# Optimization experiments

Measured on AMD Instinct MI355X. Metric: run time of the kernel, lower is better.

Reference implementation:

```python
import jax, jax.numpy as jnp
import numpy as np

N, IN_DIM, HID, HEADS, HOPS, NCLS, E = 20000, 1536, 256, 4, 3, 3, 320000
HD = HID // HEADS
EPS = 1e-5
NEG_SLOPE = 0.2


def layer_norm(x, g, b):
    mu = jnp.mean(x, axis=-1, keepdims=True)
    var = jnp.var(x, axis=-1, keepdims=True)
    return (x - mu) * jax.lax.rsqrt(var + EPS) * g + b


def gatv2(x, src, dst, Wl, bl, Wr, br, att, bias):
    # x: [N, HID]; src/dst: [E'] (self loops included)
    xl = (x @ Wl + bl).reshape(N, HEADS, HD)  # source transform
    xr = (x @ Wr + br).reshape(N, HEADS, HD)  # target transform
    e = jax.nn.leaky_relu(xl[src] + xr[dst], NEG_SLOPE)          # [E', H, D]
    logits = jnp.einsum('ehd,hd->eh', e, att)                     # [E', H]
    m = jax.ops.segment_max(logits, dst, num_segments=N)         # [N, H]
    ex = jnp.exp(logits - m[dst])
    denom = jax.ops.segment_sum(ex, dst, num_segments=N)
    alpha = ex / denom[dst]                                       # softmax per dst
    msg = xl[src] * alpha[:, :, None]                             # [E', H, D]
    out = jax.ops.segment_sum(msg, dst, num_segments=N)
    return out.reshape(N, HID) + bias


def setup_inputs() -> dict:
    key = jax.random.key(0)
    ks = jax.random.split(key, 20)
    s = lambda k, shp, sc: jax.random.normal(k, shp, jnp.float32) * sc
    return {
        'features': s(ks[0], (N, IN_DIM), 1.0),
        'edge_index': jax.random.randint(ks[1], (2, E), 0, N, jnp.int64),
        'proj_W': s(ks[2], (IN_DIM, HID), 0.02),
        'proj_b': jnp.zeros((HID,), jnp.float32),
        'n0_g': jnp.ones((HID,), jnp.float32),
        'n0_b': jnp.zeros((HID,), jnp.float32),
        'Wl': s(ks[3], (HOPS, HID, HID), 0.05),
        'bl': jnp.zeros((HOPS, HID), jnp.float32),
        'Wr': s(ks[4], (HOPS, HID, HID), 0.05),
        'br': jnp.zeros((HOPS, HID), jnp.float32),
        'att': s(ks[5], (HOPS, HEADS, HD), 0.1),
        'gbias': jnp.zeros((HOPS, HID), jnp.float32),
        'ln_g': jnp.ones((HOPS, HID), jnp.float32),
        'ln_b': jnp.zeros((HOPS, HID), jnp.float32),
        'h1_W': s(ks[6], (HID, HID), 0.05),
        'h1_b': jnp.zeros((HID,), jnp.float32),
        'h2_W': s(ks[7], (HID, NCLS), 0.05),
        'h2_b': jnp.zeros((NCLS,), jnp.float32),
    }


def reference(features, edge_index, proj_W, proj_b, n0_g, n0_b, Wl, bl, Wr, br,
              att, gbias, ln_g, ln_b, h1_W, h1_b, h2_W, h2_b):
    # add self loops (PyG GATv2Conv default)
    loop = jnp.arange(N, dtype=edge_index.dtype)
    src = jnp.concatenate([edge_index[0], loop])
    dst = jnp.concatenate([edge_index[1], loop])

    x = layer_norm(features @ proj_W + proj_b, n0_g, n0_b)
    for h in range(HOPS):
        g = gatv2(x, src, dst, Wl[h], bl[h], Wr[h], br[h], att[h], gbias[h])
        x = layer_norm(g + x, ln_g[h], ln_b[h])
    # head (dropout inactive at eval); torch GELU is exact erf form
    x = jax.nn.gelu(x @ h1_W + h1_b, approximate=False)
    return x @ h2_W + h2_b
```

## Files before the change

### kernel.cpp

```cpp
#include <hip/hip_runtime.h>
#include <hip/hip_bf16.h>
#include <math.h>

#define NN 20000
#define MPAD 20096
#define INDIM 1536
#define HID 256
#define NE 320000
#define NEDGE (NE + NN)
#define EPSV 1e-5f
#define NEG 0.2f

typedef unsigned short ushort_b;
typedef unsigned int uint32;
typedef __bf16 bf16x8 __attribute__((ext_vector_type(8)));
typedef float f32x4 __attribute__((ext_vector_type(4)));

#define AS1(p) ((const __attribute__((address_space(1))) void*)(p))
#define AS3(p) ((__attribute__((address_space(3))) void*)(p))

__device__ inline ushort_b f2bf(float x) {
  union { float f; uint32 u; } v; v.f = x;
  uint32 r = v.u + 0x7FFFu + ((v.u >> 16) & 1u);
  return (ushort_b)(r >> 16);
}
__device__ inline float bf2f(ushort_b h) {
  union { uint32 u; float f; } v; v.u = ((uint32)h) << 16;
  return v.f;
}
__device__ inline float4 ldbf4(const ushort_b* p) {
  ushort4 u = *(const ushort4*)p;
  float4 f;
  f.x = bf2f(u.x); f.y = bf2f(u.y); f.z = bf2f(u.z); f.w = bf2f(u.w);
  return f;
}

template<int AFP32, int OUTMODE, int SPLITK>
__global__ __launch_bounds__(256) void gemm_mfma(
    const void* __restrict__ Av,
    const ushort_b* __restrict__ Bt0, const ushort_b* __restrict__ Bt1,
    const float* __restrict__ bias0, const float* __restrict__ bias1,
    void* __restrict__ C0, void* __restrict__ C1,
    int Mstore, int Kloop, int Kstride)
{
  __shared__ ushort_b As0[128 * 32], As1[128 * 32];
  __shared__ ushort_b Bs0[128 * 32], Bs1[128 * 32];
  const ushort_b* Bt;
  const float* bias;
  void* Cv;
  int kbase;
  if (SPLITK > 1) {
    Bt = Bt0;
    bias = (blockIdx.z == 0) ? bias0 : nullptr;
    Cv = (float*)C0 + (size_t)blockIdx.z * NN * HID;
    kbase = blockIdx.z * Kloop;
  } else {
    Bt = blockIdx.z ? Bt1 : Bt0;
    bias = blockIdx.z ? bias1 : bias0;
    Cv = blockIdx.z ? C1 : C0;
    kbase = 0;
  }

  int tid = threadIdx.x;
  int wave = tid >> 6, lane = tid & 63;
  int r0 = blockIdx.y * 128;
  int c0 = blockIdx.x * 128;
  int wm = (wave >> 1) << 6, wn = (wave & 1) << 6;
  int mrow = lane & 15, quad = lane >> 4;
  int nk = Kloop >> 5;

  const float* Af = (const float*)Av;
  const ushort_b* Ab = (const ushort_b*)Av;

  f32x4 acc[4][4] = {};
  float4 pA0[4], pA1[4];

  auto issueB = [&](int k0, ushort_b* lds) {
#pragma unroll
    for (int it = 0; it < 2; it++) {
      int off = (wave << 10) + (it << 12) + (lane << 4);
      int row = off >> 6, colb = off & 63;
      const char* g = (const char*)Bt + ((size_t)(c0 + row) * Kstride + kbase + k0) * 2 + colb;
      __builtin_amdgcn_global_load_lds(AS1(g), AS3((char*)lds + off), 16, 0, 0);
    }
  };
  auto issueA = [&](int k0, ushort_b* lds) {
#pragma unroll
    for (int it = 0; it < 2; it++) {
      int off = (wave << 10) + (it << 12) + (lane << 4);
      int row = off >> 6, colb = off & 63;
      const char* g = (const char*)Ab + ((size_t)(r0 + row) * Kstride + kbase + k0) * 2 + colb;
      __builtin_amdgcn_global_load_lds(AS1(g), AS3((char*)lds + off), 16, 0, 0);
    }
  };
  auto loadA = [&](int k0, float4* dst) {
#pragma unroll
    for (int p = 0; p < 4; p++) {
      int off4 = (p << 8) + tid;
      int row = off4 >> 3, col4 = off4 & 7;
      int grow = r0 + row;
      dst[p] = (grow < Mstore)
          ? *(const float4*)(Af + (size_t)grow * Kstride + kbase + k0 + (col4 << 2))
          : make_float4(0.f, 0.f, 0.f, 0.f);
    }
  };
  auto writeA = [&](const float4* src, ushort_b* lds) {
#pragma unroll
    for (int p = 0; p < 4; p++) {
      int off4 = (p << 8) + tid;
      int row = off4 >> 3, col4 = off4 & 7;
      uint2 u;
      u.x = (uint32)f2bf(src[p].x) | ((uint32)f2bf(src[p].y) << 16);
      u.y = (uint32)f2bf(src[p].z) | ((uint32)f2bf(src[p].w) << 16);
      *(uint2*)(lds + (row << 5) + (col4 << 2)) = u;
    }
  };
  auto computeStage = [&](const ushort_b* Asb, const ushort_b* Bsb) {
    bf16x8 af[4], bfr[4];
#pragma unroll
    for (int t = 0; t < 4; t++) {
      af[t]  = *(const bf16x8*)(Asb + ((wm + (t << 4) + mrow) << 5) + (quad << 3));
      bfr[t] = *(const bf16x8*)(Bsb + ((wn + (t << 4) + mrow) << 5) + (quad << 3));
    }
#pragma unroll
    for (int mt = 0; mt < 4; mt++)
#pragma unroll
      for (int nt = 0; nt < 4; nt++)
        acc[mt][nt] = __builtin_amdgcn_mfma_f32_16x16x32_bf16(af[mt], bfr[nt], acc[mt][nt], 0, 0, 0);
  };

  if (AFP32) {
    loadA(0, pA0);
    issueB(0, Bs0);
    loadA(32, pA1);
    writeA(pA0, As0);
  } else {
    issueA(0, As0);
    issueB(0, Bs0);
  }

  for (int k = 0; k < nk; k += 2) {
    __syncthreads();
    if (k + 1 < nk) {
      issueB((k + 1) << 5, Bs1);
      if (AFP32) {
        writeA(pA1, As1);
        if (k + 2 < nk) loadA((k + 2) << 5, pA0);
      } else {
        issueA((k + 1) << 5, As1);
      }
    }
    computeStage(As0, Bs0);
    __syncthreads();
    if (k + 2 < nk) {
      issueB((k + 2) << 5, Bs0);
      if (AFP32) {
        writeA(pA0, As0);
        if (k + 3 < nk) loadA((k + 3) << 5, pA1);
      } else {
        issueA((k + 2) << 5, As0);
      }
    }
    computeStage(As1, Bs1);
  }

#pragma unroll
  for (int nt = 0; nt < 4; nt++) {
    int col = c0 + wn + (nt << 4) + mrow;
    float bb = bias ? bias[col] : 0.f;
#pragma unroll
    for (int mt = 0; mt < 4; mt++) {
#pragma unroll
      for (int r = 0; r < 4; r++) {
        int row = r0 + wm + (mt << 4) + (quad << 2) + r;
        if (row < Mstore) {
          float v = acc[mt][nt][r] + bb;
          if (OUTMODE == 3) v = 0.5f * v * (1.f + erff(v * 0.70710678118654752f));
          if (OUTMODE == 0) ((float*)Cv)[(size_t)row * 256 + col] = v;
          else              ((ushort_b*)Cv)[(size_t)row * 256 + col] = f2bf(v);
        }
      }
    }
  }
}

__global__ __launch_bounds__(256) void transpose_all(
    const float* __restrict__ Wl, const float* __restrict__ Wr,
    const float* __restrict__ h1W, const float* __restrict__ projW,
    ushort_b* __restrict__ wbase, ushort_b* __restrict__ wtp)
{
  __shared__ float t[32][33];
  int z = blockIdx.z;
  int tx = threadIdx.x;
  if (z < 7) {
    const float* in = (z < 3) ? Wl + (size_t)z * 65536
                    : (z < 6) ? Wr + (size_t)(z - 3) * 65536
                              : h1W;
    ushort_b* out = wbase + (size_t)z * 65536;
    int bx = blockIdx.x * 32, by = blockIdx.y * 32;
    for (int i = threadIdx.y; i < 32; i += 8)
      t[i][tx] = in[(size_t)(by + i) * 256 + bx + tx];
    __syncthreads();
    for (int i = threadIdx.y; i < 32; i += 8)
      out[(size_t)(bx + i) * 256 + by + tx] = f2bf(t[tx][i]);
  } else {
    if (blockIdx.y) return;
    int by = (z - 7) * 32;
    int bx = blockIdx.x * 32;
    for (int i = threadIdx.y; i < 32; i += 8)
      t[i][tx] = projW[(size_t)(by + i) * 256 + bx + tx];
    __syncthreads();
    for (int i = threadIdx.y; i < 32; i += 8)
      wtp[(size_t)(bx + i) * INDIM + by + tx] = f2bf(t[tx][i]);
  }
}

__global__ __launch_bounds__(256) void ln_sum4_kernel(
    const float* __restrict__ parts, const float* __restrict__ g,
    const float* __restrict__ b, float* __restrict__ out,
    ushort_b* __restrict__ bf_out)
{
  int wave = threadIdx.x >> 6, lane = threadIdx.x & 63;
  int row = blockIdx.x * 4 + wave;
  int c = lane << 2;
  if (row >= NN) {
    if (row < MPAD) *(ushort4*)(bf_out + (size_t)row * HID + c) = make_ushort4(0, 0, 0, 0);
    return;
  }
  float4 v = *(const float4*)(parts + (size_t)row * HID + c);
#pragma unroll
  for (int k = 1; k < 4; k++) {
    float4 p = *(const float4*)(parts + (size_t)k * NN * HID + (size_t)row * HID + c);
    v.x += p.x; v.y += p.y; v.z += p.z; v.w += p.w;
  }
  float s1 = v.x + v.y + v.z + v.w;
  float s2 = v.x * v.x + v.y * v.y + v.z * v.z + v.w * v.w;
#pragma unroll
  for (int m = 1; m < 64; m <<= 1) {
    s1 += __shfl_xor(s1, m, 64);
    s2 += __shfl_xor(s2, m, 64);
  }
  float mu = s1 * (1.f / 256.f);
  float var = s2 * (1.f / 256.f) - mu * mu;
  float rstd = rsqrtf(var + EPSV);
  float4 gv = *(const float4*)(g + c);
  float4 bv = *(const float4*)(b + c);
  float4 o;
  o.x = (v.x - mu) * rstd * gv.x + bv.x;
  o.y = (v.y - mu) * rstd * gv.y + bv.y;
  o.z = (v.z - mu) * rstd * gv.z + bv.z;
  o.w = (v.w - mu) * rstd * gv.w + bv.w;
  *(float4*)(out + (size_t)row * HID + c) = o;
  ushort4 ub;
  ub.x = f2bf(o.x); ub.y = f2bf(o.y); ub.z = f2bf(o.z); ub.w = f2bf(o.w);
  *(ushort4*)(bf_out + (size_t)row * HID + c) = ub;
}

__global__ void count_kernel(const int* __restrict__ ei, int* __restrict__ cnt)
{
  int e = blockIdx.x * blockDim.x + threadIdx.x;
  if (e < NEDGE) {
    int d = (e < NE) ? ei[NE + e] : (e - NE);
    atomicAdd(&cnt[d], 1);
  }
}

__global__ __launch_bounds__(1024) void scan_kernel(
    const int* __restrict__ cnt, int* __restrict__ offs, int* __restrict__ cursor)
{
  __shared__ int sums[1024];
  int tid = threadIdx.x;
  const int CH = 20;
  int base = tid * CH;
  int loc[CH];
  int s = 0;
#pragma unroll
  for (int i = 0; i < CH; i++) {
    int idx = base + i;
    int v = (idx < NN) ? cnt[idx] : 0;
    loc[i] = s;
    s += v;
  }
  sums[tid] = s;
  __syncthreads();
  for (int off = 1; off < 1024; off <<= 1) {
    int t = (tid >= off) ? sums[tid - off] : 0;
    __syncthreads();
    sums[tid] += t;
    __syncthreads();
  }
  int pre = (tid == 0) ? 0 : sums[tid - 1];
#pragma unroll
  for (int i = 0; i < CH; i++) {
    int idx = base + i;
    if (idx < NN) { int e = pre + loc[i]; offs[idx] = e; cursor[idx] = e; }
  }
  if (tid == 0) offs[NN] = NEDGE;
}

__global__ void scatter_kernel(const int* __restrict__ ei, int* __restrict__ cursor,
                               int* __restrict__ csr_src)
{
  int e = blockIdx.x * blockDim.x + threadIdx.x;
  if (e < NEDGE) {
    int s, d;
    if (e < NE) { s = ei[e]; d = ei[NE + e]; }
    else { s = e - NE; d = e - NE; }
    int p = atomicAdd(&cursor[d], 1);
    csr_src[p] = s;
  }
}

__device__ inline float edge_logit(float4 xv, float4 xrv, float4 attv) {
  float e0 = xv.x + xrv.x, e1 = xv.y + xrv.y, e2 = xv.z + xrv.z, e3 = xv.w + xrv.w;
  e0 = (e0 > 0.f) ? e0 : NEG * e0;
  e1 = (e1 > 0.f) ? e1 : NEG * e1;
  e2 = (e2 > 0.f) ? e2 : NEG * e2;
  e3 = (e3 > 0.f) ? e3 : NEG * e3;
  float lc = e0 * attv.x + e1 * attv.y + e2 * attv.z + e3 * attv.w;
  lc += __shfl_xor(lc, 1, 16);
  lc += __shfl_xor(lc, 2, 16);
  lc += __shfl_xor(lc, 4, 16);
  lc += __shfl_xor(lc, 8, 16);
  return lc;
}

#define ACCUM(i, lg, xv) {                          \
    float w = __expf(lg);                            \
    lS[i] += w;                                      \
    pS##i##0 += w * xv.x; pS##i##1 += w * xv.y;      \
    pS##i##2 += w * xv.z; pS##i##3 += w * xv.w; }

__global__ __launch_bounds__(256) void gat_kernel(
    const ushort_b* __restrict__ xl, const ushort_b* __restrict__ xr,
    const float* __restrict__ x_in, const float* __restrict__ att,
    const float* __restrict__ gbias, const float* __restrict__ ln_g,
    const float* __restrict__ ln_b, const int* __restrict__ offs,
    const int* __restrict__ csr_src, float* __restrict__ x_out,
    ushort_b* __restrict__ xb_out)
{
  __shared__ float gbuf[2][64][5];
  int wave = threadIdx.x >> 6, lane = threadIdx.x & 63;
  int nib = wave >> 1, sub = wave & 1;
  int node = blockIdx.x * 2 + nib;
  int c = lane << 2;
  float4 xrv = ldbf4(xr + (size_t)node * HID + c);
  float4 attv = *(const float4*)(att + c);

  float lS[4] = {0.f, 0.f, 0.f, 0.f};
  float pS00 = 0.f, pS01 = 0.f, pS02 = 0.f, pS03 = 0.f;
  float pS10 = 0.f, pS11 = 0.f, pS12 = 0.f, pS13 = 0.f;
  float pS20 = 0.f, pS21 = 0.f, pS22 = 0.f, pS23 = 0.f;
  float pS30 = 0.f, pS31 = 0.f, pS32 = 0.f, pS33 = 0.f;

  int beg = offs[node], end = offs[node + 1];
  int mid = beg + ((end - beg + 1) >> 1);
  int e  = sub ? mid : beg;
  int e1 = sub ? end : mid;
  for (; e + 3 < e1; e += 4) {
    int s0 = csr_src[e], s1 = csr_src[e + 1], s2 = csr_src[e + 2], s3 = csr_src[e + 3];
    float4 x0v = ldbf4(xl + (size_t)s0 * HID + c);
    float4 x1v = ldbf4(xl + (size_t)s1 * HID + c);
    float4 x2v = ldbf4(xl + (size_t)s2 * HID + c);
    float4 x3v = ldbf4(xl + (size_t)s3 * HID + c);
    float g0 = edge_logit(x0v, xrv, attv);
    float g1 = edge_logit(x1v, xrv, attv);
    float g2 = edge_logit(x2v, xrv, attv);
    float g3 = edge_logit(x3v, xrv, attv);
    ACCUM(0, g0, x0v);
    ACCUM(1, g1, x1v);
    ACCUM(2, g2, x2v);
    ACCUM(3, g3, x3v);
  }
  for (; e < e1; e++) {
    int s0 = csr_src[e];
    float4 x0v = ldbf4(xl + (size_t)s0 * HID + c);
    float g0 = edge_logit(x0v, xrv, attv);
    ACCUM(0, g0, x0v);
  }

  float l  = lS[0] + lS[1] + lS[2] + lS[3];
  float q0 = pS00 + pS10 + pS20 + pS30;
  float q1 = pS01 + pS11 + pS21 + pS31;
  float q2 = pS02 + pS12 + pS22 + pS32;
  float q3 = pS03 + pS13 + pS23 + pS33;

  if (sub) {
    gbuf[nib][lane][0] = l;
    gbuf[nib][lane][1] = q0;
    gbuf[nib][lane][2] = q1;
    gbuf[nib][lane][3] = q2;
    gbuf[nib][lane][4] = q3;
  }
  __syncthreads();
  if (sub) return;

  l  += gbuf[nib][lane][0];
  q0 += gbuf[nib][lane][1];
  q1 += gbuf[nib][lane][2];
  q2 += gbuf[nib][lane][3];
  q3 += gbuf[nib][lane][4];

  float inv = 1.f / l;
  float4 xv = *(const float4*)(x_in + (size_t)node * HID + c);
  float4 gb = *(const float4*)(gbias + c);
  float o0 = q0 * inv + gb.x + xv.x;
  float o1 = q1 * inv + gb.y + xv.y;
  float o2 = q2 * inv + gb.z + xv.z;
  float o3 = q3 * inv + gb.w + xv.w;
  float s1s = o0 + o1 + o2 + o3;
  float s2s = o0 * o0 + o1 * o1 + o2 * o2 + o3 * o3;
#pragma unroll
  for (int mmk = 1; mmk < 64; mmk <<= 1) {
    s1s += __shfl_xor(s1s, mmk, 64);
    s2s += __shfl_xor(s2s, mmk, 64);
  }
  float mu = s1s * (1.f / 256.f);
  float var = s2s * (1.f / 256.f) - mu * mu;
  float rstd = rsqrtf(var + EPSV);
  float4 gv = *(const float4*)(ln_g + c);
  float4 bv = *(const float4*)(ln_b + c);
  float4 o;
  o.x = (o0 - mu) * rstd * gv.x + bv.x;
  o.y = (o1 - mu) * rstd * gv.y + bv.y;
  o.z = (o2 - mu) * rstd * gv.z + bv.z;
  o.w = (o3 - mu) * rstd * gv.w + bv.w;
  *(float4*)(x_out + (size_t)node * HID + c) = o;
  ushort4 ub;
  ub.x = f2bf(o.x); ub.y = f2bf(o.y); ub.z = f2bf(o.z); ub.w = f2bf(o.w);
  *(ushort4*)(xb_out + (size_t)node * HID + c) = ub;
}

__global__ __launch_bounds__(256) void head2_kernel(
    const ushort_b* __restrict__ t1, const float* __restrict__ W,
    const float* __restrict__ bias, float* __restrict__ out)
{
  int wave = threadIdx.x >> 6, lane = threadIdx.x & 63;
  int row = blockIdx.x * 4 + wave;
  if (row >= NN) return;
  int c = lane << 2;
  float4 v = ldbf4(t1 + (size_t)row * HID + c);
  float p0 = 0.f, p1 = 0.f, p2 = 0.f;
#pragma unroll
  for (int j = 0; j < 4; j++) {
    float vj = (&v.x)[j];
    p0 += vj * W[(c + j) * 3 + 0];
    p1 += vj * W[(c + j) * 3 + 1];
    p2 += vj * W[(c + j) * 3 + 2];
  }
#pragma unroll
  for (int mm = 1; mm < 64; mm <<= 1) {
    p0 += __shfl_xor(p0, mm, 64);
    p1 += __shfl_xor(p1, mm, 64);
    p2 += __shfl_xor(p2, mm, 64);
  }
  if (lane == 0) {
    out[(size_t)row * 3 + 0] = p0 + bias[0];
    out[(size_t)row * 3 + 1] = p1 + bias[1];
    out[(size_t)row * 3 + 2] = p2 + bias[2];
  }
}

extern "C" void kernel_launch(void* const* d_in, const int* in_sizes, int n_in,
                              void* d_out, int out_size, void* d_ws, size_t ws_size,
                              hipStream_t stream)
{
  const float* features = (const float*)d_in[0];
  const int*   ei       = (const int*)d_in[1];
  const float* proj_W   = (const float*)d_in[2];
  const float* proj_b   = (const float*)d_in[3];
  const float* n0_g     = (const float*)d_in[4];
  const float* n0_b     = (const float*)d_in[5];
  const float* Wl       = (const float*)d_in[6];
  const float* bl       = (const float*)d_in[7];
  const float* Wr       = (const float*)d_in[8];
  const float* br       = (const float*)d_in[9];
  const float* att      = (const float*)d_in[10];
  const float* gbias    = (const float*)d_in[11];
  const float* ln_g     = (const float*)d_in[12];
  const float* ln_b     = (const float*)d_in[13];
  const float* h1_W     = (const float*)d_in[14];
  const float* h1_b     = (const float*)d_in[15];
  const float* h2_W     = (const float*)d_in[16];
  const float* h2_b     = (const float*)d_in[17];
  float* out = (float*)d_out;

  char* w = (char*)d_ws;
  float*    x0    = (float*)w;    w += (size_t)NN * HID * 4;
  float*    x1    = (float*)w;    w += (size_t)NN * HID * 4;
  float*    part1 = (float*)w;    w += (size_t)NN * HID * 4;
  ushort_b* xlb   = (ushort_b*)w; w += (size_t)NN * HID * 2;
  ushort_b* xrb   = (ushort_b*)w; w += (size_t)NN * HID * 2;
  ushort_b* xb    = (ushort_b*)w; w += (size_t)MPAD * HID * 2;
  ushort_b* wtp   = (ushort_b*)w; w += (size_t)HID * INDIM * 2;
  ushort_b* wtl   = (ushort_b*)w; w += (size_t)3 * HID * HID * 2;
  ushort_b* wtr   = (ushort_b*)w; w += (size_t)3 * HID * HID * 2;
  ushort_b* wth1  = (ushort_b*)w; w += (size_t)HID * HID * 2;
  int* cnt     = (int*)w;  w += (size_t)NN * 4;
  int* offs    = (int*)w;  w += (size_t)(NN + 1) * 4;
  int* cursor  = (int*)w;  w += (size_t)NN * 4;
  int* csr     = (int*)w;  w += (size_t)NEDGE * 4;
  (void)part1;

  hipMemsetAsync(cnt, 0, (size_t)NN * 4, stream);
  count_kernel<<<(NEDGE + 255) / 256, 256, 0, stream>>>(ei, cnt);
  scan_kernel<<<1, 1024, 0, stream>>>(cnt, offs, cursor);
  scatter_kernel<<<(NEDGE + 255) / 256, 256, 0, stream>>>(ei, cursor, csr);

  transpose_all<<<dim3(8, 8, 55), dim3(32, 8), 0, stream>>>(Wl, Wr, h1_W, proj_W, wtl, wtp);

  dim3 gproj(2, MPAD / 128, 4);
  dim3 ghop(2, MPAD / 128, 2);
  dim3 gone(2, MPAD / 128, 1);

  gemm_mfma<1, 0, 4><<<gproj, 256, 0, stream>>>(
      features, wtp, nullptr, proj_b, nullptr, x0, nullptr, NN, INDIM / 4, INDIM);
  ln_sum4_kernel<<<MPAD / 4, 256, 0, stream>>>(x0, n0_g, n0_b, x0, xb);

  float* xcur = x0;
  float* xnxt = x1;
  for (int h = 0; h < 3; h++) {
    gemm_mfma<0, 2, 1><<<ghop, 256, 0, stream>>>(
        xb, wtl + (size_t)h * HID * HID, wtr + (size_t)h * HID * HID,
        bl + h * HID, br + h * HID, xlb, xrb, NN, HID, HID);
    gat_kernel<<<NN / 2, 256, 0, stream>>>(
        xlb, xrb, xcur, att + h * HID, gbias + h * HID,
        ln_g + h * HID, ln_b + h * HID, offs, csr, xnxt, xb);
    float* t = xcur; xcur = xnxt; xnxt = t;
  }

  gemm_mfma<0, 3, 1><<<gone, 256, 0, stream>>>(
      xb, wth1, wth1, h1_b, h1_b, xlb, xlb, NN, HID, HID);
  head2_kernel<<<(NN + 3) / 4, 256, 0, stream>>>(xlb, h2_W, h2_b, out);
}
```

Measured before the change: 570.9 us.

## Replace pipelined GEMM with B-resident LDS kernel and direct global A fragments

The double-buffered 128x128 GEMM is replaced by a kernel that loads a 64-column slab of the transposed weights for its whole K range into LDS once. Each wave then reads its A fragments straight from global memory into registers, converting fp32 to bf16 inline for the projection, so there is no A staging in LDS and no per-step barriers. The projection split-K drops from 4 parts to 3 (K=512 each) with a matching 3-part layernorm reduction, and blocks grow to 512 threads covering 256 rows. The cost is that A loads go uncoalesced from global memory with no latency-hiding pipeline, and the projection kernel now holds 64 KB of LDS per block, which may limit occupancy.

```diff
diff --git a/kernel.cpp b/kernel.cpp
--- a/kernel.cpp
+++ b/kernel.cpp
@@ -35,146 +35,107 @@
   return f;
 }
 
-template<int AFP32, int OUTMODE, int SPLITK>
-__global__ __launch_bounds__(256) void gemm_mfma(
+template<int AFP32, int OUTMODE, int KSZ, int MODE>
+__global__ __launch_bounds__(512) void gemm_bres(
     const void* __restrict__ Av,
     const ushort_b* __restrict__ Bt0, const ushort_b* __restrict__ Bt1,
     const float* __restrict__ bias0, const float* __restrict__ bias1,
     void* __restrict__ C0, void* __restrict__ C1,
-    int Mstore, int Kloop, int Kstride)
-{
-  __shared__ ushort_b As0[128 * 32], As1[128 * 32];
-  __shared__ ushort_b Bs0[128 * 32], Bs1[128 * 32];
+    int Mstore, int Kstride)
+{
+  __shared__ ushort_b Bs[64 * KSZ];
   const ushort_b* Bt;
   const float* bias;
   void* Cv;
-  int kbase;
-  if (SPLITK > 1) {
+  int kbase, c0;
+  if (MODE == 0) {
     Bt = Bt0;
     bias = (blockIdx.z == 0) ? bias0 : nullptr;
     Cv = (float*)C0 + (size_t)blockIdx.z * NN * HID;
-    kbase = blockIdx.z * Kloop;
+    kbase = blockIdx.z * KSZ;
+    c0 = blockIdx.x * 64;
+  } else if (MODE == 1) {
+    int mat = blockIdx.x >> 2;
+    Bt = mat ? Bt1 : Bt0;
+    bias = mat ? bias1 : bias0;
+    Cv = mat ? C1 : C0;
+    kbase = 0;
+    c0 = (blockIdx.x & 3) * 64;
   } else {
-    Bt = blockIdx.z ? Bt1 : Bt0;
-    bias = blockIdx.z ? bias1 : bias0;
-    Cv = blockIdx.z ? C1 : C0;
+    Bt = Bt0; bias = bias0; Cv = C0;
     kbase = 0;
+    c0 = blockIdx.x * 64;
   }
 
   int tid = threadIdx.x;
+
+  constexpr int NB = (64 * KSZ * 2) / (512 * 16);
+#pragma unroll
+  for (int i = 0; i < NB; i++) {
+    int byte = (tid + i * 512) << 4;
+    int kc = byte >> 12;
+    int within = byte & 4095;
+    int ccol = within >> 6;
+    int kb = within & 63;
+    const char* g = (const char*)Bt + (size_t)(c0 + ccol) * Kstride * 2
+                  + (size_t)(kbase + kc * 32) * 2 + kb;
+    __builtin_amdgcn_global_load_lds(AS1(g), AS3((char*)Bs + byte), 16, 0, 0);
+  }
+  __syncthreads();
+
   int wave = tid >> 6, lane = tid & 63;
-  int r0 = blockIdx.y * 128;
-  int c0 = blockIdx.x * 128;
-  int wm = (wave >> 1) << 6, wn = (wave & 1) << 6;
+  int msub = wave >> 1, nsub = wave & 1;
   int mrow = lane & 15, quad = lane >> 4;
-  int nk = Kloop >> 5;
+  int r0t = blockIdx.y * 256 + msub * 64;
+  if (r0t >= Mstore) return;
 
   const float* Af = (const float*)Av;
   const ushort_b* Ab = (const ushort_b*)Av;
 
-  f32x4 acc[4][4] = {};
-  float4 pA0[4], pA1[4];
-
-  auto issueB = [&](int k0, ushort_b* lds) {
-#pragma unroll
-    for (int it = 0; it < 2; it++) {
-      int off = (wave << 10) + (it << 12) + (lane << 4);
-      int row = off >> 6, colb = off & 63;
-      const char* g = (const char*)Bt + ((size_t)(c0 + row) * Kstride + kbase + k0) * 2 + colb;
-      __builtin_amdgcn_global_load_lds(AS1(g), AS3((char*)lds + off), 16, 0, 0);
-    }
-  };
-  auto issueA = [&](int k0, ushort_b* lds) {
-#pragma unroll
-    for (int it = 0; it < 2; it++) {
-      int off = (wave << 10) + (it << 12) + (lane << 4);
-      int row = off >> 6, colb = off & 63;
-      const char* g = (const char*)Ab + ((size_t)(r0 + row) * Kstride + kbase + k0) * 2 + colb;
-      __builtin_amdgcn_global_load_lds(AS1(g), AS3((char*)lds + off), 16, 0, 0);
-    }
-  };
-  auto loadA = [&](int k0, float4* dst) {
-#pragma unroll
-    for (int p = 0; p < 4; p++) {
-      int off4 = (p << 8) + tid;
-      int row = off4 >> 3, col4 = off4 & 7;
-      int grow = r0 + row;
-      dst[p] = (grow < Mstore)
-          ? *(const float4*)(Af + (size_t)grow * Kstride + kbase + k0 + (col4 << 2))
-          : make_float4(0.f, 0.f, 0.f, 0.f);
-    }
-  };
-  auto writeA = [&](const float4* src, ushort_b* lds) {
-#pragma unroll
-    for (int p = 0; p < 4; p++) {
-      int off4 = (p << 8) + tid;
-      int row = off4 >> 3, col4 = off4 & 7;
-      uint2 u;
-      u.x = (uint32)f2bf(src[p].x) | ((uint32)f2bf(src[p].y) << 16);
-      u.y = (uint32)f2bf(src[p].z) | ((uint32)f2bf(src[p].w) << 16);
-      *(uint2*)(lds + (row << 5) + (col4 << 2)) = u;
-    }
-  };
-  auto computeStage = [&](const ushort_b* Asb, const ushort_b* Bsb) {
-    bf16x8 af[4], bfr[4];
+  f32x4 acc[4][2] = {};
+#pragma unroll
+  for (int kc = 0; kc < KSZ / 32; kc++) {
+    bf16x8 af[4];
 #pragma unroll
     for (int t = 0; t < 4; t++) {
-      af[t]  = *(const bf16x8*)(Asb + ((wm + (t << 4) + mrow) << 5) + (quad << 3));
-      bfr[t] = *(const bf16x8*)(Bsb + ((wn + (t << 4) + mrow) << 5) + (quad << 3));
-    }
-#pragma unroll
-    for (int mt = 0; mt < 4; mt++)
-#pragma unroll
-      for (int nt = 0; nt < 4; nt++)
-        acc[mt][nt] = __builtin_amdgcn_mfma_f32_16x16x32_bf16(af[mt], bfr[nt], acc[mt][nt], 0, 0, 0);
-  };
-
-  if (AFP32) {
-    loadA(0, pA0);
-    issueB(0, Bs0);
-    loadA(32, pA1);
-    writeA(pA0, As0);
-  } else {
-    issueA(0, As0);
-    issueB(0, Bs0);
-  }
-
-  for (int k = 0; k < nk; k += 2) {
-    __syncthreads();
-    if (k + 1 < nk) {
-      issueB((k + 1) << 5, Bs1);
+      int grow = r0t + (t << 4) + mrow;
       if (AFP32) {
-        writeA(pA1, As1);
-        if (k + 2 < nk) loadA((k + 2) << 5, pA0);
+        int gr = grow < Mstore ? grow : Mstore - 1;
+        const float* p = Af + (size_t)gr * Kstride + kbase + (kc << 5) + (quad << 3);
+        float4 u0 = *(const float4*)p;
+        float4 u1 = *(const float4*)(p + 4);
+        union { bf16x8 v; uint32 u[4]; } pk;
+        pk.u[0] = (uint32)f2bf(u0.x) | ((uint32)f2bf(u0.y) << 16);
+        pk.u[1] = (uint32)f2bf(u0.z) | ((uint32)f2bf(u0.w) << 16);
+        pk.u[2] = (uint32)f2bf(u1.x) | ((uint32)f2bf(u1.y) << 16);
+        pk.u[3] = (uint32)f2bf(u1.z) | ((uint32)f2bf(u1.w) << 16);
+        af[t] = pk.v;
       } else {
-        issueA((k + 1) << 5, As1);
+        af[t] = *(const bf16x8*)(Ab + (size_t)grow * Kstride + (kc << 5) + (quad << 3));
       }
     }
-    computeStage(As0, Bs0);
-    __syncthreads();
-    if (k + 2 < nk) {
-      issueB((k + 2) << 5, Bs0);
-      if (AFP32) {
-        writeA(pA0, As0);
-        if (k + 3 < nk) loadA((k + 3) << 5, pA1);
-      } else {
-        issueA((k + 2) << 5, As0);
-      }
-    }
-    computeStage(As1, Bs1);
-  }
-
-#pragma unroll
-  for (int nt = 0; nt < 4; nt++) {
-    int col = c0 + wn + (nt << 4) + mrow;
+    bf16x8 bfr[2];
+#pragma unroll
+    for (int u = 0; u < 2; u++)
+      bfr[u] = *(const bf16x8*)(Bs + kc * 2048 + ((nsub << 5) + (u << 4) + mrow) * 32 + (quad << 3));
+#pragma unroll
+    for (int t = 0; t < 4; t++)
+#pragma unroll
+      for (int u = 0; u < 2; u++)
+        acc[t][u] = __builtin_amdgcn_mfma_f32_16x16x32_bf16(af[t], bfr[u], acc[t][u], 0, 0, 0);
+  }
+
+#pragma unroll
+  for (int u = 0; u < 2; u++) {
+    int col = c0 + (nsub << 5) + (u << 4) + mrow;
     float bb = bias ? bias[col] : 0.f;
 #pragma unroll
-    for (int mt = 0; mt < 4; mt++) {
+    for (int t = 0; t < 4; t++) {
 #pragma unroll
       for (int r = 0; r < 4; r++) {
-        int row = r0 + wm + (mt << 4) + (quad << 2) + r;
+        int row = r0t + (t << 4) + (quad << 2) + r;
         if (row < Mstore) {
-          float v = acc[mt][nt][r] + bb;
+          float v = acc[t][u][r] + bb;
           if (OUTMODE == 3) v = 0.5f * v * (1.f + erff(v * 0.70710678118654752f));
           if (OUTMODE == 0) ((float*)Cv)[(size_t)row * 256 + col] = v;
           else              ((ushort_b*)Cv)[(size_t)row * 256 + col] = f2bf(v);
@@ -215,7 +176,7 @@
   }
 }
 
-__global__ __launch_bounds__(256) void ln_sum4_kernel(
+__global__ __launch_bounds__(256) void ln_sum3_kernel(
     const float* __restrict__ parts, const float* __restrict__ g,
     const float* __restrict__ b, float* __restrict__ out,
     ushort_b* __restrict__ bf_out)
@@ -229,7 +190,7 @@
   }
   float4 v = *(const float4*)(parts + (size_t)row * HID + c);
 #pragma unroll
-  for (int k = 1; k < 4; k++) {
+  for (int k = 1; k < 3; k++) {
     float4 p = *(const float4*)(parts + (size_t)k * NN * HID + (size_t)row * HID + c);
     v.x += p.x; v.y += p.y; v.z += p.z; v.w += p.w;
   }
@@ -488,7 +449,7 @@
   char* w = (char*)d_ws;
   float*    x0    = (float*)w;    w += (size_t)NN * HID * 4;
   float*    x1    = (float*)w;    w += (size_t)NN * HID * 4;
-  float*    part1 = (float*)w;    w += (size_t)NN * HID * 4;
+  float*    part2 = (float*)w;    w += (size_t)NN * HID * 4;
   ushort_b* xlb   = (ushort_b*)w; w += (size_t)NN * HID * 2;
   ushort_b* xrb   = (ushort_b*)w; w += (size_t)NN * HID * 2;
   ushort_b* xb    = (ushort_b*)w; w += (size_t)MPAD * HID * 2;
@@ -500,7 +461,7 @@
   int* offs    = (int*)w;  w += (size_t)(NN + 1) * 4;
   int* cursor  = (int*)w;  w += (size_t)NN * 4;
   int* csr     = (int*)w;  w += (size_t)NEDGE * 4;
-  (void)part1;
+  (void)part2;
 
   hipMemsetAsync(cnt, 0, (size_t)NN * 4, stream);
   count_kernel<<<(NEDGE + 255) / 256, 256, 0, stream>>>(ei, cnt);
@@ -509,27 +470,25 @@
 
   transpose_all<<<dim3(8, 8, 55), dim3(32, 8), 0, stream>>>(Wl, Wr, h1_W, proj_W, wtl, wtp);
 
-  dim3 gproj(2, MPAD / 128, 4);
-  dim3 ghop(2, MPAD / 128, 2);
-  dim3 gone(2, MPAD / 128, 1);
-
-  gemm_mfma<1, 0, 4><<<gproj, 256, 0, stream>>>(
-      features, wtp, nullptr, proj_b, nullptr, x0, nullptr, NN, INDIM / 4, INDIM);
-  ln_sum4_kernel<<<MPAD / 4, 256, 0, stream>>>(x0, n0_g, n0_b, x0, xb);
+  const int GY = (MPAD + 255) / 256;
+
+  gemm_bres<1, 0, 512, 0><<<dim3(4, GY, 3), 512, 0, stream>>>(
+      features, wtp, nullptr, proj_b, nullptr, x0, nullptr, NN, INDIM);
+  ln_sum3_kernel<<<MPAD / 4, 256, 0, stream>>>(x0, n0_g, n0_b, x0, xb);
 
   float* xcur = x0;
   float* xnxt = x1;
   for (int h = 0; h < 3; h++) {
-    gemm_mfma<0, 2, 1><<<ghop, 256, 0, stream>>>(
+    gemm_bres<0, 2, 256, 1><<<dim3(8, GY, 1), 512, 0, stream>>>(
         xb, wtl + (size_t)h * HID * HID, wtr + (size_t)h * HID * HID,
-        bl + h * HID, br + h * HID, xlb, xrb, NN, HID, HID);
+        bl + h * HID, br + h * HID, xlb, xrb, NN, HID);
     gat_kernel<<<NN / 2, 256, 0, stream>>>(
         xlb, xrb, xcur, att + h * HID, gbias + h * HID,
         ln_g + h * HID, ln_b + h * HID, offs, csr, xnxt, xb);
     float* t = xcur; xcur = xnxt; xnxt = t;
   }
 
-  gemm_mfma<0, 3, 1><<<gone, 256, 0, stream>>>(
-      xb, wth1, wth1, h1_b, h1_b, xlb, xlb, NN, HID, HID);
+  gemm_bres<0, 3, 256, 2><<<dim3(4, GY, 1), 512, 0, stream>>>(
+      xb, wth1, nullptr, h1_b, nullptr, xlb, nullptr, NN, HID);
   head2_kernel<<<(NN + 3) / 4, 256, 0, stream>>>(xlb, h2_W, h2_b, out);
 }
```

After: 650.3 us. 13.9% more time.
